# Optimization experiments

Measured on AMD Instinct MI355X. Metric: run time of the kernel, lower is better.

Reference implementation:

```python
import jax, jax.numpy as jnp
import numpy as np

N, H, CIN, C, G = 50000, 16, 256, 256, 8
CPG = C // G          # 32 channels per group
CR = C // 4           # delta MLP hidden (delta_reduction=4)

def _lrelu(x):
    return jax.nn.leaky_relu(x, 0.1)

def setup_inputs() -> dict:
    key = jax.random.key(0)
    ks = jax.random.split(key, 16)
    def lin(k, fin, fout):
        return jax.random.normal(k, (fin, fout), jnp.float32) / np.sqrt(fin)
    return {
        'q_pts': jax.random.normal(ks[0], (N, 3), jnp.float32),
        's_pts': jax.random.normal(ks[1], (N, 3), jnp.float32),
        's_feats': jax.random.normal(ks[2], (N, CIN), jnp.float32),
        'neighb_inds': jax.random.randint(ks[3], (N, H), 0, N, jnp.int64),
        'Wq': lin(ks[4], CIN, C), 'bq': jnp.zeros((C,), jnp.float32),
        'Wk': lin(ks[5], CIN, C), 'bk': jnp.zeros((C,), jnp.float32),
        'Wv': lin(ks[6], CIN, C), 'bv': jnp.zeros((C,), jnp.float32),
        'Wd1': lin(ks[7], 3, CR), 'bd1': jnp.zeros((CR,), jnp.float32),
        'Wd2': lin(ks[8], CR, C), 'bd2': jnp.zeros((C,), jnp.float32),
        'Wa1': lin(ks[9], C, CPG), 'ba1': jnp.zeros((CPG,), jnp.float32),
        'Wa2': lin(ks[10], CPG, CPG), 'ba2': jnp.zeros((CPG,), jnp.float32),
    }

def reference(q_pts, s_pts, s_feats, neighb_inds,
              Wq, bq, Wk, bk, Wv, bv,
              Wd1, bd1, Wd2, bd2, Wa1, ba1, Wa2, ba2):
    # q/k/v projections  (N, C)
    v = s_feats @ Wv + bv
    k = s_feats @ Wk + bk
    q = s_feats @ Wq + bq
    # gather neighbor features (all indices < N, shadow mask is a no-op)
    nv = v[neighb_inds]                 # (N, H, C)
    nk = k[neighb_inds]                 # (N, H, C)
    # relative positions (torch.no_grad in source)
    rel = s_pts[neighb_inds] - q_pts[:, None, :]   # (N, H, 3)
    # delta MLP: 3 -> C/4 -> C (UnaryBlock + Linear, norm='none')
    geom = _lrelu(rel @ Wd1 + bd1) @ Wd2 + bd2     # (N, H, C)
    # geom_mode='sub': v-branch and qk-branch both subtract geom encodings
    nv = nv - geom
    # source always enters strided branch (s_pts padded before the check);
    # stride_mode='nearest' -> q feature of the first neighbor
    qf = q[neighb_inds[:, 0]]                      # (N, C)
    qk = qf[:, None, :] - nk - geom                # (N, H, C)
    # alpha MLP: NormBlock(id) + act, Linear C->CpG + act, Linear CpG->CpG
    a = _lrelu(qk)
    a = _lrelu(a @ Wa1 + ba1)
    a = a @ Wa2 + ba2                              # (N, H, CpG)
    attn = jax.nn.softmax(a, axis=1)               # softmax over neighbors
    # grouped weighted aggregation: C split as (CpG, G), attn broadcast over G
    out = (nv.reshape(N, H, CPG, G) * attn[..., None]).sum(axis=1)
    return out.reshape(N, C)
```

## Files before the change

### kernel.cpp

```cpp
#include <hip/hip_runtime.h>
#include <cstdint>
#include <cstddef>

#define N_PTS 50000
#define H 16
#define CIN 256
#define C 256
#define CPG 32
#define CR 64

typedef short bf16x8 __attribute__((ext_vector_type(8)));
typedef float f32x4 __attribute__((ext_vector_type(4)));

__device__ __forceinline__ unsigned short f2bf(float f) {
    __bf16 b = (__bf16)f;
    return __builtin_bit_cast(unsigned short, b);
}
__device__ __forceinline__ float bf2f(unsigned short s) {
    return __uint_as_float(((unsigned int)s) << 16);
}

__global__ __launch_bounds__(256) void prep_all(
    const float* __restrict__ Wq, const float* __restrict__ Wk,
    const float* __restrict__ Wv,
    const float* __restrict__ Wd2, const float* __restrict__ Wa1,
    const float* __restrict__ Wa2,
    unsigned short* __restrict__ gemmFrags,
    unsigned short* __restrict__ attnFrags)
{
    int bid = blockIdx.x;
    if (bid < 96) {
        int t = bid * 256 + threadIdx.x;
        int lane = t & 63;
        int f = t >> 6;
        int ntg = f % 48;
        const float* W = ntg < 16 ? Wq : (ntg < 32 ? Wk : Wv);
        int colc = (ntg & 15) * 16 + (lane & 15);
        int row0 = (f / 48) * 32 + ((lane >> 4) << 3);
        unsigned short tmp[8];
        #pragma unroll
        for (int j = 0; j < 8; ++j) tmp[j] = f2bf(W[(size_t)(row0 + j) * 256 + colc]);
        *(bf16x8*)&gemmFrags[(size_t)t * 8] = *(bf16x8*)tmp;
    } else {
        int t = (bid - 96) * 256 + threadIdx.x;
        if (t >= 3200) return;
        const float* W; int Nc, NT, loc, base;
        if (t < 2048)      { W = Wd2; Nc = 256; NT = 16; loc = t;        base = 0; }
        else if (t < 3072) { W = Wa1; Nc = 32;  NT = 2;  loc = t - 2048; base = 16384; }
        else               { W = Wa2; Nc = 32;  NT = 2;  loc = t - 3072; base = 24576; }
        int f = loc >> 6, lane = loc & 63;
        int kt = f / NT, nt = f - kt * NT;
        int colc = nt * 16 + (lane & 15);
        int row0 = kt * 32 + ((lane >> 4) << 3);
        unsigned short tmp[8];
        #pragma unroll
        for (int j = 0; j < 8; ++j) tmp[j] = f2bf(W[(size_t)(row0 + j) * Nc + colc]);
        *(bf16x8*)&attnFrags[(size_t)(base + loc * 8)] = *(bf16x8*)tmp;
    }
}

__global__ __launch_bounds__(256) void qkv_gemm_mfma(
    const float* __restrict__ feats,
    const unsigned short* __restrict__ wfrags,
    const float* __restrict__ bq, const float* __restrict__ bk,
    const float* __restrict__ bv, unsigned short* __restrict__ out)
{
    __shared__ unsigned short s_b[64 * 64 * 8];
    const int tid = threadIdx.x;
    const int lane = tid & 63, wave = tid >> 6;
    const int quad = lane >> 4, col16 = lane & 15;
    const int bx = blockIdx.x, by = blockIdx.y;
    const bool kvmode = bx >= 2;
    const int qd = bx - 2;

    #pragma unroll
    for (int i = 0; i < 16; ++i) {
        int ci = i * 256 + tid;
        int f = ci >> 6, w = ci & 63;
        int kt = f >> 3, nt = f & 7;
        int ntg = !kvmode ? (bx * 8 + nt)
                          : (nt < 4 ? (16 + qd * 4 + nt) : (32 + qd * 4 + nt - 4));
        *(bf16x8*)&s_b[(size_t)ci * 8] =
            *(const bf16x8*)&wfrags[((size_t)(kt * 48 + ntg) * 64 + w) * 8];
    }

    int r0 = by * 128 + wave * 32 + col16;
    int r1 = r0 + 16;
    r0 = r0 < N_PTS ? r0 : N_PTS - 1;
    r1 = r1 < N_PTS ? r1 : N_PTS - 1;
    const float* a0p = &feats[(size_t)r0 * 256 + quad * 8];
    const float* a1p = &feats[(size_t)r1 * 256 + quad * 8];

    f32x4 acc[2][8] = {};
    __syncthreads();

    #pragma unroll 2
    for (int kt = 0; kt < 8; ++kt) {
        float4 f00 = *(const float4*)(a0p + kt * 32);
        float4 f01 = *(const float4*)(a0p + kt * 32 + 4);
        float4 f10 = *(const float4*)(a1p + kt * 32);
        float4 f11 = *(const float4*)(a1p + kt * 32 + 4);
        unsigned short t0[8] = {f2bf(f00.x), f2bf(f00.y), f2bf(f00.z), f2bf(f00.w),
                                f2bf(f01.x), f2bf(f01.y), f2bf(f01.z), f2bf(f01.w)};
        unsigned short t1[8] = {f2bf(f10.x), f2bf(f10.y), f2bf(f10.z), f2bf(f10.w),
                                f2bf(f11.x), f2bf(f11.y), f2bf(f11.z), f2bf(f11.w)};
        bf16x8 af0 = *(bf16x8*)t0;
        bf16x8 af1 = *(bf16x8*)t1;
        #pragma unroll
        for (int nt = 0; nt < 8; ++nt) {
            bf16x8 bf = *(bf16x8*)&s_b[((kt * 8 + nt) * 64 + lane) * 8];
            acc[0][nt] = __builtin_amdgcn_mfma_f32_16x16x32_bf16(af0, bf, acc[0][nt], 0, 0, 0);
            acc[1][nt] = __builtin_amdgcn_mfma_f32_16x16x32_bf16(af1, bf, acc[1][nt], 0, 0, 0);
        }
    }

    if (!kvmode) {
        #pragma unroll
        for (int nt = 0; nt < 8; ++nt) {
            int cIn = bx * 128 + nt * 16 + col16;
            float bb = bq[cIn];
            #pragma unroll
            for (int mt = 0; mt < 2; ++mt) {
                #pragma unroll
                for (int r = 0; r < 4; ++r) {
                    int row = by * 128 + wave * 32 + mt * 16 + quad * 4 + r;
                    if (row < N_PTS)
                        out[(size_t)row * 768 + cIn] = f2bf(acc[mt][nt][r] + bb);
                }
            }
        }
    } else {
        unsigned int* out32 = (unsigned int*)out;
        #pragma unroll
        for (int nt = 0; nt < 4; ++nt) {
            int cIn = qd * 64 + nt * 16 + col16;
            float bbk = bk[cIn], bbv = bv[cIn];
            #pragma unroll
            for (int mt = 0; mt < 2; ++mt) {
                #pragma unroll
                for (int r = 0; r < 4; ++r) {
                    int row = by * 128 + wave * 32 + mt * 16 + quad * 4 + r;
                    if (row < N_PTS) {
                        unsigned int kk = f2bf(acc[mt][nt][r] + bbk);
                        unsigned int vv = f2bf(acc[mt][nt + 4][r] + bbv);
                        out32[(size_t)row * 384 + 128 + cIn] = kk | (vv << 16);
                    }
                }
            }
        }
    }
}

#define D1S 72
#define PGS 66
#define QKS 264
#define A1S 40
#define A2S 33

__global__ __launch_bounds__(256) void attn_mfma(
    const unsigned short* __restrict__ qkv,
    const float* __restrict__ q_pts, const float* __restrict__ s_pts,
    const int* __restrict__ nbr,
    const float* __restrict__ Wd1, const float* __restrict__ bd1,
    const float* __restrict__ bd2,
    const unsigned short* __restrict__ frags,
    const float* __restrict__ ba1, const float* __restrict__ ba2,
    float* __restrict__ out)
{
    __shared__ unsigned short s_d1[H * D1S];
    __shared__ float          s_pg[4 * H * PGS];
    __shared__ unsigned short s_qk[H * QKS];
    __shared__ unsigned short s_a1[H * A1S];
    __shared__ float          s_a2[H * A2S];
    __shared__ float          s_rel[4][H][3];
    __shared__ int            s_idx[4][H];

    const int tid = threadIdx.x;
    const int lane = tid & 63, wave = tid >> 6;
    const int quad = lane >> 4, col = lane & 15;
    const int n0 = blockIdx.x * 4;
    const int c = tid;

    if (tid < 64) {
        int pp = tid >> 4, hh = tid & 15;
        int idx = nbr[(size_t)(n0 + pp) * H + hh];
        s_idx[pp][hh] = idx;
        #pragma unroll
        for (int x = 0; x < 3; ++x)
            s_rel[pp][hh][x] = s_pts[(size_t)idx * 3 + x] - q_pts[(size_t)(n0 + pp) * 3 + x];
    }

    const float w1x = Wd1[lane], w1y = Wd1[64 + lane], w1z = Wd1[128 + lane];
    const float b1 = bd1[lane];
    const float b2 = bd2[c];
    bf16x8 wd2f[2][4];
    #pragma unroll
    for (int t = 0; t < 4; ++t) {
        wd2f[0][t] = *(const bf16x8*)&frags[((size_t)((0 * 16 + wave * 4 + t) * 64 + lane)) * 8];
        wd2f[1][t] = *(const bf16x8*)&frags[((size_t)((1 * 16 + wave * 4 + t) * 64 + lane)) * 8];
    }
    bf16x8 wa1f[8];
    bf16x8 wa2f = {0,0,0,0,0,0,0,0};
    if (wave < 2) {
        #pragma unroll
        for (int kt = 0; kt < 8; ++kt)
            wa1f[kt] = *(const bf16x8*)&frags[16384 + ((size_t)((kt * 2 + wave) * 64 + lane)) * 8];
        wa2f = *(const bf16x8*)&frags[24576 + ((size_t)(wave * 64 + lane)) * 8];
    }
    __syncthreads();

    float* pg = &s_pg[wave * (H * PGS)];

    for (int p = 0; p < 4; ++p) {
        const int n = n0 + p;

        #pragma unroll
        for (int pass = 0; pass < 4; ++pass) {
            int h = pass * 4 + wave;
            float v = b1 + s_rel[p][h][0] * w1x + s_rel[p][h][1] * w1y + s_rel[p][h][2] * w1z;
            s_d1[h * D1S + lane] = f2bf(fmaxf(v, 0.1f * v));
        }
        __syncthreads();

        unsigned int u[H];
        #pragma unroll
        for (int h = 0; h < H; ++h)
            u[h] = *(const unsigned int*)&qkv[(size_t)s_idx[p][h] * 768 + 256 + 2 * c];
        float qf = bf2f(qkv[(size_t)s_idx[p][0] * 768 + c]);

        {
            bf16x8 ga = *(bf16x8*)&s_d1[col * D1S + quad * 8];
            bf16x8 gb = *(bf16x8*)&s_d1[col * D1S + 32 + quad * 8];
            #pragma unroll
            for (int t = 0; t < 4; ++t) {
                f32x4 acc = {0.f, 0.f, 0.f, 0.f};
                acc = __builtin_amdgcn_mfma_f32_16x16x32_bf16(ga, wd2f[0][t], acc, 0, 0, 0);
                acc = __builtin_amdgcn_mfma_f32_16x16x32_bf16(gb, wd2f[1][t], acc, 0, 0, 0);
                #pragma unroll
                for (int rr = 0; rr < 4; ++rr)
                    pg[(quad * 4 + rr) * PGS + t * 16 + col] = acc[rr];
            }
        }

        float vg[H];
        #pragma unroll
        for (int h = 0; h < H; ++h) {
            float g = pg[h * PGS + lane] + b2;
            float nk = __uint_as_float(u[h] << 16);
            float nv = __uint_as_float(u[h] & 0xffff0000u);
            vg[h] = nv - g;
            float tq = qf - nk - g;
            s_qk[h * QKS + c] = f2bf(fmaxf(tq, 0.1f * tq));
        }
        __syncthreads();

        if (wave < 2) {
            f32x4 acc = {0.f, 0.f, 0.f, 0.f};
            #pragma unroll
            for (int kt = 0; kt < 8; ++kt) {
                bf16x8 a = *(bf16x8*)&s_qk[col * QKS + kt * 32 + quad * 8];
                acc = __builtin_amdgcn_mfma_f32_16x16x32_bf16(a, wa1f[kt], acc, 0, 0, 0);
            }
            int j = wave * 16 + col;
            float bb = ba1[j];
            #pragma unroll
            for (int rr = 0; rr < 4; ++rr) {
                float v = acc[rr] + bb;
                s_a1[(quad * 4 + rr) * A1S + j] = f2bf(fmaxf(v, 0.1f * v));
            }
        }
        __syncthreads();

        if (wave < 2) {
            bf16x8 aa = *(bf16x8*)&s_a1[col * A1S + quad * 8];
            f32x4 acc = {0.f, 0.f, 0.f, 0.f};
            acc = __builtin_amdgcn_mfma_f32_16x16x32_bf16(aa, wa2f, acc, 0, 0, 0);
            int j = wave * 16 + col;
            float bb = ba2[j];
            #pragma unroll
            for (int rr = 0; rr < 4; ++rr)
                s_a2[(quad * 4 + rr) * A2S + j] = acc[rr] + bb;
        }
        __syncthreads();

        if (wave == 0) {
            int j = lane & 31, hb = (lane >> 5) * 8;
            float vals[8];
            float mx = -1e30f;
            #pragma unroll
            for (int i = 0; i < 8; ++i) {
                vals[i] = s_a2[(hb + i) * A2S + j];
                mx = fmaxf(mx, vals[i]);
            }
            mx = fmaxf(mx, __shfl_xor(mx, 32));
            float sum = 0.f;
            #pragma unroll
            for (int i = 0; i < 8; ++i) { vals[i] = __expf(vals[i] - mx); sum += vals[i]; }
            sum += __shfl_xor(sum, 32);
            float inv = 1.f / sum;
            #pragma unroll
            for (int i = 0; i < 8; ++i) s_a2[(hb + i) * A2S + j] = vals[i] * inv;
        }
        __syncthreads();

        float o = 0.f;
        const int aj = c >> 3;
        #pragma unroll
        for (int h = 0; h < H; ++h) o += vg[h] * s_a2[h * A2S + aj];
        out[(size_t)n * C + c] = o;
    }
}


extern "C" void kernel_launch(void* const* d_in, const int* in_sizes, int n_in,
                              void* d_out, int out_size, void* d_ws, size_t ws_size,
                              hipStream_t stream) {
    const float* q_pts   = (const float*)d_in[0];
    const float* s_pts   = (const float*)d_in[1];
    const float* s_feats = (const float*)d_in[2];
    const int*   nbr     = (const int*)d_in[3];
    const float* Wq  = (const float*)d_in[4];
    const float* bq  = (const float*)d_in[5];
    const float* Wk  = (const float*)d_in[6];
    const float* bk  = (const float*)d_in[7];
    const float* Wv  = (const float*)d_in[8];
    const float* bv  = (const float*)d_in[9];
    const float* Wd1 = (const float*)d_in[10];
    const float* bd1 = (const float*)d_in[11];
    const float* Wd2 = (const float*)d_in[12];
    const float* bd2 = (const float*)d_in[13];
    const float* Wa1 = (const float*)d_in[14];
    const float* ba1 = (const float*)d_in[15];
    const float* Wa2 = (const float*)d_in[16];
    const float* ba2 = (const float*)d_in[17];

    float* out = (float*)d_out;
    char* ws = (char*)d_ws;
    unsigned short* qkvb      = (unsigned short*)(ws + 25600000);
    unsigned short* attnFrags = (unsigned short*)(ws + 102400000);
    unsigned short* gemmFrags = (unsigned short*)(ws + 102451200);

    prep_all<<<109, 256, 0, stream>>>(Wq, Wk, Wv, Wd2, Wa1, Wa2,
                                      gemmFrags, attnFrags);

    dim3 g1(6, (N_PTS + 127) / 128);
    qkv_gemm_mfma<<<g1, 256, 0, stream>>>(s_feats, gemmFrags, bq, bk, bv, qkvb);

    attn_mfma<<<(N_PTS / 4), 256, 0, stream>>>(qkvb, q_pts, s_pts, nbr,
                                               Wd1, bd1, bd2, attnFrags,
                                               ba1, ba2, out);
}
```

Before: 414.9 us.

## Pre-convert features to bf16 fragments and retile QKV GEMM with staged LDS

Measured after the change: 375.7 us. 1.1x faster.

```diff
diff --git a/kernel.cpp b/kernel.cpp
--- a/kernel.cpp
+++ b/kernel.cpp
@@ -20,17 +20,35 @@
     return __uint_as_float(((unsigned int)s) << 16);
 }
 
+#define LBAR() do { asm volatile("s_waitcnt lgkmcnt(0)" ::: "memory"); \
+                    __builtin_amdgcn_s_barrier();                      \
+                    asm volatile("" ::: "memory"); } while (0)
+
 __global__ __launch_bounds__(256) void prep_all(
+    const float* __restrict__ feats,
     const float* __restrict__ Wq, const float* __restrict__ Wk,
     const float* __restrict__ Wv,
     const float* __restrict__ Wd2, const float* __restrict__ Wa1,
     const float* __restrict__ Wa2,
+    unsigned short* __restrict__ Afrag,
     unsigned short* __restrict__ gemmFrags,
     unsigned short* __restrict__ attnFrags)
 {
     int bid = blockIdx.x;
-    if (bid < 96) {
+    if (bid < 6250) {
         int t = bid * 256 + threadIdx.x;
+        int lane = t & 63, f = t >> 6;
+        int R2 = f >> 3, kt = f & 7;
+        int row = R2 * 16 + (lane & 15);
+        int col = kt * 32 + ((lane >> 4) << 3);
+        const float* s = &feats[(size_t)row * 256 + col];
+        float4 f0 = *(const float4*)s;
+        float4 f1 = *(const float4*)(s + 4);
+        unsigned short tmp[8] = {f2bf(f0.x), f2bf(f0.y), f2bf(f0.z), f2bf(f0.w),
+                                 f2bf(f1.x), f2bf(f1.y), f2bf(f1.z), f2bf(f1.w)};
+        *(bf16x8*)&Afrag[(size_t)t * 8] = *(bf16x8*)tmp;
+    } else if (bid < 6346) {
+        int t = (bid - 6250) * 256 + threadIdx.x;
         int lane = t & 63;
         int f = t >> 6;
         int ntg = f % 48;
@@ -42,7 +60,7 @@
         for (int j = 0; j < 8; ++j) tmp[j] = f2bf(W[(size_t)(row0 + j) * 256 + colc]);
         *(bf16x8*)&gemmFrags[(size_t)t * 8] = *(bf16x8*)tmp;
     } else {
-        int t = (bid - 96) * 256 + threadIdx.x;
+        int t = (bid - 6346) * 256 + threadIdx.x;
         if (t >= 3200) return;
         const float* W; int Nc, NT, loc, base;
         if (t < 2048)      { W = Wd2; Nc = 256; NT = 16; loc = t;        base = 0; }
@@ -60,90 +78,110 @@
 }
 
 __global__ __launch_bounds__(256) void qkv_gemm_mfma(
-    const float* __restrict__ feats,
+    const unsigned short* __restrict__ Afrag,
     const unsigned short* __restrict__ wfrags,
     const float* __restrict__ bq, const float* __restrict__ bk,
     const float* __restrict__ bv, unsigned short* __restrict__ out)
 {
-    __shared__ unsigned short s_b[64 * 64 * 8];
+    __shared__ unsigned short s_ab[16 * 64 * 8];
     const int tid = threadIdx.x;
     const int lane = tid & 63, wave = tid >> 6;
     const int quad = lane >> 4, col16 = lane & 15;
+    const int wr = wave >> 1, wc = wave & 1;
     const int bx = blockIdx.x, by = blockIdx.y;
     const bool kvmode = bx >= 2;
     const int qd = bx - 2;
 
+    const unsigned short* srcp[4];
     #pragma unroll
-    for (int i = 0; i < 16; ++i) {
-        int ci = i * 256 + tid;
-        int f = ci >> 6, w = ci & 63;
-        int kt = f >> 3, nt = f & 7;
-        int ntg = !kvmode ? (bx * 8 + nt)
-                          : (nt < 4 ? (16 + qd * 4 + nt) : (32 + qd * 4 + nt - 4));
-        *(bf16x8*)&s_b[(size_t)ci * 8] =
-            *(const bf16x8*)&wfrags[((size_t)(kt * 48 + ntg) * 64 + w) * 8];
-    }
-
-    int r0 = by * 128 + wave * 32 + col16;
-    int r1 = r0 + 16;
-    r0 = r0 < N_PTS ? r0 : N_PTS - 1;
-    r1 = r1 < N_PTS ? r1 : N_PTS - 1;
-    const float* a0p = &feats[(size_t)r0 * 256 + quad * 8];
-    const float* a1p = &feats[(size_t)r1 * 256 + quad * 8];
-
-    f32x4 acc[2][8] = {};
-    __syncthreads();
-
-    #pragma unroll 2
+    for (int i = 0; i < 4; ++i) {
+        int c = wave * 4 + i;
+        if (c < 8) {
+            int R2 = by * 8 + c;
+            R2 = R2 < 3125 ? R2 : 3124;
+            srcp[i] = &Afrag[(((size_t)R2 * 8) * 64 + lane) * 8];
+        } else {
+            int nt = c - 8;
+            int ntg;
+            if (!kvmode) ntg = bx * 8 + nt;
+            else {
+                int cf = nt >> 1;
+                ntg = ((nt & 1) ? 32 : 16) + qd * 4 + cf;
+            }
+            srcp[i] = &wfrags[((size_t)ntg * 64 + lane) * 8];
+        }
+    }
+    const int sstep = (wave < 2) ? 512 : 24576;
+    unsigned short* dstp = &s_ab[((wave * 4) * 64 + lane) * 8];
+    const unsigned short* afp = &s_ab[((wr * 4) * 64 + lane) * 8];
+    const unsigned short* bfp = &s_ab[((8 + wc * 4) * 64 + lane) * 8];
+
+    bf16x8 cur[4], nxt[4];
+    #pragma unroll
+    for (int i = 0; i < 4; ++i) cur[i] = *(const bf16x8*)(srcp[i]);
+
+    f32x4 acc[4][4] = {};
+
+    #pragma unroll
     for (int kt = 0; kt < 8; ++kt) {
-        float4 f00 = *(const float4*)(a0p + kt * 32);
-        float4 f01 = *(const float4*)(a0p + kt * 32 + 4);
-        float4 f10 = *(const float4*)(a1p + kt * 32);
-        float4 f11 = *(const float4*)(a1p + kt * 32 + 4);
-        unsigned short t0[8] = {f2bf(f00.x), f2bf(f00.y), f2bf(f00.z), f2bf(f00.w),
-                                f2bf(f01.x), f2bf(f01.y), f2bf(f01.z), f2bf(f01.w)};
-        unsigned short t1[8] = {f2bf(f10.x), f2bf(f10.y), f2bf(f10.z), f2bf(f10.w),
-                                f2bf(f11.x), f2bf(f11.y), f2bf(f11.z), f2bf(f11.w)};
-        bf16x8 af0 = *(bf16x8*)t0;
-        bf16x8 af1 = *(bf16x8*)t1;
-        #pragma unroll
-        for (int nt = 0; nt < 8; ++nt) {
-            bf16x8 bf = *(bf16x8*)&s_b[((kt * 8 + nt) * 64 + lane) * 8];
-            acc[0][nt] = __builtin_amdgcn_mfma_f32_16x16x32_bf16(af0, bf, acc[0][nt], 0, 0, 0);
-            acc[1][nt] = __builtin_amdgcn_mfma_f32_16x16x32_bf16(af1, bf, acc[1][nt], 0, 0, 0);
+        #pragma unroll
+        for (int i = 0; i < 4; ++i)
+            *(bf16x8*)(dstp + i * 512) = cur[i];
+        if (kt < 7) {
+            #pragma unroll
+            for (int i = 0; i < 4; ++i)
+                nxt[i] = *(const bf16x8*)(srcp[i] + (size_t)(kt + 1) * sstep);
+        }
+        LBAR();
+        bf16x8 af[4], bf[4];
+        #pragma unroll
+        for (int m = 0; m < 4; ++m) af[m] = *(const bf16x8*)(afp + m * 512);
+        #pragma unroll
+        for (int n = 0; n < 4; ++n) bf[n] = *(const bf16x8*)(bfp + n * 512);
+        #pragma unroll
+        for (int m = 0; m < 4; ++m)
+            #pragma unroll
+            for (int n = 0; n < 4; ++n)
+                acc[m][n] = __builtin_amdgcn_mfma_f32_16x16x32_bf16(af[m], bf[n], acc[m][n], 0, 0, 0);
+        LBAR();
+        if (kt < 7) {
+            #pragma unroll
+            for (int i = 0; i < 4; ++i) cur[i] = nxt[i];
         }
     }
 
     if (!kvmode) {
         #pragma unroll
-        for (int nt = 0; nt < 8; ++nt) {
-            int cIn = bx * 128 + nt * 16 + col16;
-            float bb = bq[cIn];
-            #pragma unroll
-            for (int mt = 0; mt < 2; ++mt) {
+        for (int n = 0; n < 4; ++n) {
+            int col = bx * 128 + (wc * 4 + n) * 16 + col16;
+            float bb = bq[col];
+            #pragma unroll
+            for (int m = 0; m < 4; ++m) {
+                int rbase = by * 128 + (wr * 4 + m) * 16 + quad * 4;
                 #pragma unroll
                 for (int r = 0; r < 4; ++r) {
-                    int row = by * 128 + wave * 32 + mt * 16 + quad * 4 + r;
+                    int row = rbase + r;
                     if (row < N_PTS)
-                        out[(size_t)row * 768 + cIn] = f2bf(acc[mt][nt][r] + bb);
+                        out[(size_t)row * 768 + col] = f2bf(acc[m][n][r] + bb);
                 }
             }
         }
     } else {
         unsigned int* out32 = (unsigned int*)out;
         #pragma unroll
-        for (int nt = 0; nt < 4; ++nt) {
-            int cIn = qd * 64 + nt * 16 + col16;
-            float bbk = bk[cIn], bbv = bv[cIn];
-            #pragma unroll
-            for (int mt = 0; mt < 2; ++mt) {
+        for (int cf = 0; cf < 2; ++cf) {
+            int col = qd * 64 + (wc * 2 + cf) * 16 + col16;
+            float bbk = bk[col], bbv = bv[col];
+            #pragma unroll
+            for (int m = 0; m < 4; ++m) {
+                int rbase = by * 128 + (wr * 4 + m) * 16 + quad * 4;
                 #pragma unroll
                 for (int r = 0; r < 4; ++r) {
-                    int row = by * 128 + wave * 32 + mt * 16 + quad * 4 + r;
+                    int row = rbase + r;
                     if (row < N_PTS) {
-                        unsigned int kk = f2bf(acc[mt][nt][r] + bbk);
-                        unsigned int vv = f2bf(acc[mt][nt + 4][r] + bbv);
-                        out32[(size_t)row * 384 + 128 + cIn] = kk | (vv << 16);
+                        unsigned int kk = f2bf(acc[m][2 * cf][r] + bbk);
+                        unsigned int vv = f2bf(acc[m][2 * cf + 1][r] + bbv);
+                        out32[(size_t)row * 384 + 128 + col] = kk | (vv << 16);
                     }
                 }
             }
@@ -336,15 +374,16 @@
 
     float* out = (float*)d_out;
     char* ws = (char*)d_ws;
+    unsigned short* Afrag     = (unsigned short*)(ws);
     unsigned short* qkvb      = (unsigned short*)(ws + 25600000);
     unsigned short* attnFrags = (unsigned short*)(ws + 102400000);
     unsigned short* gemmFrags = (unsigned short*)(ws + 102451200);
 
-    prep_all<<<109, 256, 0, stream>>>(Wq, Wk, Wv, Wd2, Wa1, Wa2,
-                                      gemmFrags, attnFrags);
+    prep_all<<<6359, 256, 0, stream>>>(s_feats, Wq, Wk, Wv, Wd2, Wa1, Wa2,
+                                       Afrag, gemmFrags, attnFrags);
 
     dim3 g1(6, (N_PTS + 127) / 128);
-    qkv_gemm_mfma<<<g1, 256, 0, stream>>>(s_feats, gemmFrags, bq, bk, bv, qkvb);
+    qkv_gemm_mfma<<<g1, 256, 0, stream>>>(Afrag, gemmFrags, bq, bk, bv, qkvb);
 
     attn_mfma<<<(N_PTS / 4), 256, 0, stream>>>(qkvb, q_pts, s_pts, nbr,
                                                Wd1, bd1, bd2, attnFrags,
```
